# Performance work log

Measured on AMD Instinct MI355X. Metric: run time of the kernel, lower is better.

## Reference

```python
import jax, jax.numpy as jnp
import numpy as np
import math

N_S = 4096
N_T = 4096
R = 0.05
SIGMA = 0.2
K = 100.0
T = 1.0
S_MAX = 300.0
B = 100.0
ALPHA_STR = 30.0
CHI = 6.0
LAMBDA_PDE = 1.0
LAMBDA_BC = 10.0
LAMBDA_TC = 10.0
HUBER_DELTA = 0.01
ALPHA = 2.0 * R / SIGMA ** 2            # 2r/sigma^2
TAU_MAX = 0.5 * SIGMA ** 2 * T
DU = 1.0 / (N_S - 1)                     # dS_norm for the S-stencils
DT_NORM = TAU_MAX / (N_T - 1)            # dt_norm for the t-stencil


def _solve_depressed_cubic(Q):
    # Faithful port of CubicStretching._solve_depressed_cubic (hyperbolic root formula).
    p = CHI
    q = CHI * Q
    sp = math.sqrt(p)
    arg = abs(q) / (2.0 * p * sp / (3.0 * math.sqrt(3.0)))
    arg = max(1.0, arg)
    c = 2.0 * sp * math.cosh(math.acosh(arg) / 3.0)
    return -c if q >= 0 else c


C1 = _solve_depressed_cubic((B - 0.0) / ALPHA_STR)
C2 = _solve_depressed_cubic((B - S_MAX) / ALPHA_STR)


def _stretch_metrics(u):
    # CubicStretching.compute_metrics: S(u), dS/du, d2S/du2.
    L = C2 * u + C1 * (1.0 - u)
    dL = C2 - C1
    S = B + ALPHA_STR * (L ** 3 / CHI + L)
    dS = ALPHA_STR * dL * (0.5 * L ** 2 + 1.0)
    d2S = ALPHA_STR * dL ** 2 * L
    return S, dS, d2S


def setup_inputs() -> dict:
    key = jax.random.key(0)
    V_norm = 0.1 * jax.random.normal(key, (1, 1, N_S, N_T), dtype=jnp.float32)
    return {"V_norm": V_norm}


def reference(V_norm):
    # u-grid along S (axis 2), t-grid along time (axis 3)
    u = jnp.linspace(0.0, 1.0, N_S, dtype=jnp.float32)[None, None, :, None]  # [1,1,N_S,1]
    t = jnp.linspace(0.0, 1.0, N_T, dtype=jnp.float32)                       # [N_T]

    S_phys, S_u, S_uu = _stretch_metrics(u)
    S_norm = S_phys / S_MAX       # stretched physical coordinate, normalized
    S_u_n = S_u / S_MAX
    S_uu_n = S_uu / S_MAX

    # FD stencils: (3,1) central diff / second diff along S, (1,3) central diff along t,
    # all with replicate padding (= torch padding_mode='replicate').
    Vp = jnp.pad(V_norm, ((0, 0), (0, 0), (1, 1), (0, 0)), mode='edge')
    V_u = (Vp[:, :, 2:, :] - Vp[:, :, :-2, :]) / (2.0 * DU)
    V_uu = (Vp[:, :, 2:, :] - 2.0 * V_norm + Vp[:, :, :-2, :]) / DU ** 2
    Vt = jnp.pad(V_norm, ((0, 0), (0, 0), (0, 0), (1, 1)), mode='edge')
    V_t = (Vt[:, :, :, 2:] - Vt[:, :, :, :-2]) / (2.0 * DT_NORM)

    # Chain rule from uniform u to stretched S
    V_S = V_u / S_u_n
    V_SS = (V_uu * S_u_n - V_u * S_uu_n) / S_u_n ** 3
    V_SS = jnp.clip(V_SS, -100.0, 100.0)

    residual = V_t - S_norm ** 2 * V_SS - ALPHA * S_norm * V_S + ALPHA * V_norm
    # interior mask = relu(1 - S0 - Smax - T - t0) == strict interior of the grid
    n_int = (N_S - 2) * (N_T - 2)
    pde_loss = jnp.sum(residual[:, :, 1:-1, 1:-1] ** 2) / n_int

    # far-field BC at S = S_max (row N_S-1): call option -> 1 - K exp(-r(1-t))/S_max
    bc_target = 1.0 - K * jnp.exp(-R * (1.0 - t)) / S_MAX
    loss_Smax = jnp.sum((V_norm[0, 0, -1, :] - bc_target) ** 2) / N_T

    # terminal condition at t = T (col N_t-1): softplus payoff on the UNIFORM u grid
    # (forward rebinds S_norm = self.S_grid_norm before calling terminal_payoff)
    payoff = jax.nn.softplus(50.0 * (u[0, 0, :, 0] - K / S_MAX)) / 50.0
    diff_T = V_norm[0, 0, :, -1] - payoff
    abs_d = jnp.abs(diff_T)
    loss_T = jnp.sum(jnp.where(abs_d < HUBER_DELTA,
                               0.5 * diff_T ** 2,
                               HUBER_DELTA * (abs_d - 0.5 * HUBER_DELTA))) / N_S

    total = LAMBDA_PDE * pde_loss + LAMBDA_BC * loss_Smax + LAMBDA_TC * loss_T
    return total
```

## Files before the change

kernel.cpp:

```cpp
#include <hip/hip_runtime.h>
#include <math.h>

#define NS 4096
#define NT 4096
#define RPB 4
#define NBLK (NS / RPB)

__device__ __forceinline__ double block_reduce(double v, int tid) {
    #pragma unroll
    for (int off = 32; off > 0; off >>= 1)
        v += __shfl_down(v, off, 64);
    __shared__ double lds[4];
    const int lane = tid & 63, wv = tid >> 6;
    if (lane == 0) lds[wv] = v;
    __syncthreads();
    return lds[0] + lds[1] + lds[2] + lds[3];
}

__device__ __forceinline__ void load16(const float* __restrict__ p, float* d) {
    const float4 x0 = *(const float4*)(p);
    const float4 x1 = *(const float4*)(p + 4);
    const float4 x2 = *(const float4*)(p + 8);
    const float4 x3 = *(const float4*)(p + 12);
    d[0]=x0.x; d[1]=x0.y; d[2]=x0.z;  d[3]=x0.w;
    d[4]=x1.x; d[5]=x1.y; d[6]=x1.z;  d[7]=x1.w;
    d[8]=x2.x; d[9]=x2.y; d[10]=x2.z; d[11]=x2.w;
    d[12]=x3.x;d[13]=x3.y;d[14]=x3.z; d[15]=x3.w;
}

__global__ __launch_bounds__(256) void bs_main(const float* __restrict__ V,
                                               double* __restrict__ part,
                                               double C1, double C2) {
    const int tid = threadIdx.x;
    const int r0  = blockIdx.x * RPB;
    const int j0  = tid * 16;

    const double DU = 1.0 / (double)(NS - 1);
    const double dL = C2 - C1;

    const float INV2DU = 2047.5f;
    const float INVDU2 = 16769025.0f;
    const float INV2DT = 102375.0f;
    const float AL     = 2.5f;

    float a[16], b[16], c[16];
    const int rm = (r0 > 0) ? r0 - 1 : 0;
    load16(V + (size_t)rm * NT + j0, a);
    load16(V + (size_t)r0 * NT + j0, b);

    double pde = 0.0, bc = 0.0, tc = 0.0;

    #pragma unroll
    for (int rr = 0; rr < RPB; ++rr) {
        const int r  = r0 + rr;
        const int rn = (r + 1 < NS) ? r + 1 : NS - 1;
        load16(V + (size_t)rn * NT + j0, c);

        const double u   = (double)r * DU;
        const double L   = C2 * u + C1 * (1.0 - u);
        const double S   = 100.0 + 30.0 * (L * L * L / 6.0 + L);
        const double dS  = 30.0 * dL * (0.5 * L * L + 1.0);
        const double d2S = 30.0 * dL * dL * L;
        const float Sn   = (float)(S   / 300.0);
        const float Sun  = (float)(dS  / 300.0);
        const float Suun = (float)(d2S / 300.0);
        const float invSun  = 1.0f / Sun;
        const float invSun3 = invSun * invSun * invSun;
        const float Sn2 = Sn * Sn;
        const float ASn = AL * Sn;

        if (r >= 1 && r <= NS - 2) {
            const float lf = (j0 > 0)       ? V[(size_t)r * NT + j0 - 1]  : 0.0f;
            const float rt = (j0 + 16 < NT) ? V[(size_t)r * NT + j0 + 16] : 0.0f;

            float pf = 0.0f;
            #pragma unroll
            for (int k = 0; k < 16; ++k) {
                const int j = j0 + k;
                if (j >= 1 && j <= NT - 2) {
                    const float cm = (k == 0)  ? lf : b[k - 1];
                    const float cp = (k == 15) ? rt : b[k + 1];
                    const float Vu  = (c[k] - a[k]) * INV2DU;
                    const float Vuu = (c[k] - 2.0f * b[k] + a[k]) * INVDU2;
                    const float Vt  = (cp - cm) * INV2DT;
                    const float VS  = Vu * invSun;
                    float VSS = (Vuu * Sun - Vu * Suun) * invSun3;
                    VSS = fminf(fmaxf(VSS, -100.0f), 100.0f);
                    const float res = Vt - Sn2 * VSS - ASn * VS + AL * b[k];
                    pf += res * res;
                }
            }
            pde += (double)pf;
        }

        if (r == NS - 1) {
            #pragma unroll
            for (int k = 0; k < 16; ++k) {
                const float t   = (float)(j0 + k) * (1.0f / (float)(NT - 1));
                const float tgt = 1.0f - (100.0f / 300.0f) * expf(-0.05f * (1.0f - t));
                const float d   = b[k] - tgt;
                bc += (double)(d * d);
            }
        }

        if (tid == 255) {
            const float ui = (float)u;
            const float x  = 50.0f * (ui - 100.0f / 300.0f);
            const float sp = fmaxf(x, 0.0f) + log1pf(expf(-fabsf(x)));
            const float payoff = sp * (1.0f / 50.0f);
            const float d  = b[15] - payoff;
            const float ad = fabsf(d);
            tc += (double)((ad < 0.01f) ? 0.5f * d * d : 0.01f * (ad - 0.005f));
        }

        #pragma unroll
        for (int k = 0; k < 16; ++k) { a[k] = b[k]; b[k] = c[k]; }
    }

    const double n_int = (double)(NS - 2) * (double)(NT - 2);
    double contrib = pde * (1.0 / n_int)
                   + bc  * (10.0 / (double)NT)
                   + tc  * (10.0 / (double)NS);

    contrib = block_reduce(contrib, tid);
    if (tid == 0) part[blockIdx.x] = contrib;
}

__global__ __launch_bounds__(256) void bs_final(const double* __restrict__ part,
                                                float* __restrict__ out) {
    const int tid = threadIdx.x;
    double s = 0.0;
    for (int idx = tid; idx < NBLK; idx += 256) s += part[idx];
    s = block_reduce(s, tid);
    if (tid == 0) out[0] = (float)s;
}

static double cubic_root_host(double Q) {
    const double p = 6.0;
    const double q = p * Q;
    const double sp = sqrt(p);
    double arg = fabs(q) / (2.0 * p * sp / (3.0 * sqrt(3.0)));
    if (arg < 1.0) arg = 1.0;
    const double c = 2.0 * sp * cosh(acosh(arg) / 3.0);
    return (q >= 0.0) ? -c : c;
}

extern "C" void kernel_launch(void* const* d_in, const int* in_sizes, int n_in,
                              void* d_out, int out_size, void* d_ws, size_t ws_size,
                              hipStream_t stream) {
    const float* V  = (const float*)d_in[0];
    float* out      = (float*)d_out;
    double* part    = (double*)d_ws;

    const double C1 = cubic_root_host((100.0 - 0.0)   / 30.0);
    const double C2 = cubic_root_host((100.0 - 300.0) / 30.0);

    bs_main <<<NBLK, 256, 0, stream>>>(V, part, C1, C2);
    bs_final<<<1,    256, 0, stream>>>(part, out);
}
```

Measured before the change: 100.1 us.

## Split columns across blocks and fuse final reduction via last-block atomic counter

Each block now covers 8 rows and half of the columns, with 8 columns per thread instead of 16, so the grid stays at 1024 blocks while each thread holds less register data. The separate final reduction kernel is replaced by a last-block-done pattern using an atomic counter, with the counter reset by a memset before launch. This removes one kernel launch but adds a memset node and the serialized tail reduction in the last block. Halo loads per element rise slightly because each thread's column span is narrower.

New measurement: 125.4 us. +25.2%, slower.

```diff
diff --git a/kernel.cpp b/kernel.cpp
--- a/kernel.cpp
+++ b/kernel.cpp
@@ -3,8 +3,10 @@
 
 #define NS 4096
 #define NT 4096
-#define RPB 4
-#define NBLK (NS / RPB)
+#define RPB 8
+#define CCH 2048
+#define CPT 8
+#define NBLK ((NS / RPB) * (NT / CCH))
 
 __device__ __forceinline__ double block_reduce(double v, int tid) {
     #pragma unroll
@@ -17,23 +19,23 @@
     return lds[0] + lds[1] + lds[2] + lds[3];
 }
 
-__device__ __forceinline__ void load16(const float* __restrict__ p, float* d) {
+__device__ __forceinline__ void load8(const float* __restrict__ p, float* d) {
     const float4 x0 = *(const float4*)(p);
     const float4 x1 = *(const float4*)(p + 4);
-    const float4 x2 = *(const float4*)(p + 8);
-    const float4 x3 = *(const float4*)(p + 12);
-    d[0]=x0.x; d[1]=x0.y; d[2]=x0.z;  d[3]=x0.w;
-    d[4]=x1.x; d[5]=x1.y; d[6]=x1.z;  d[7]=x1.w;
-    d[8]=x2.x; d[9]=x2.y; d[10]=x2.z; d[11]=x2.w;
-    d[12]=x3.x;d[13]=x3.y;d[14]=x3.z; d[15]=x3.w;
+    d[0]=x0.x; d[1]=x0.y; d[2]=x0.z; d[3]=x0.w;
+    d[4]=x1.x; d[5]=x1.y; d[6]=x1.z; d[7]=x1.w;
 }
 
 __global__ __launch_bounds__(256) void bs_main(const float* __restrict__ V,
                                                double* __restrict__ part,
+                                               unsigned* __restrict__ cnt,
+                                               float* __restrict__ out,
                                                double C1, double C2) {
     const int tid = threadIdx.x;
-    const int r0  = blockIdx.x * RPB;
-    const int j0  = tid * 16;
+    const int rg  = blockIdx.x >> 1;
+    const int cc  = blockIdx.x & 1;
+    const int r0  = rg * RPB;
+    const int j0  = cc * CCH + tid * CPT;
 
     const double DU = 1.0 / (double)(NS - 1);
     const double dL = C2 - C1;
@@ -43,10 +45,10 @@
     const float INV2DT = 102375.0f;
     const float AL     = 2.5f;
 
-    float a[16], b[16], c[16];
+    float a[CPT], b[CPT], c[CPT];
     const int rm = (r0 > 0) ? r0 - 1 : 0;
-    load16(V + (size_t)rm * NT + j0, a);
-    load16(V + (size_t)r0 * NT + j0, b);
+    load8(V + (size_t)rm * NT + j0, a);
+    load8(V + (size_t)r0 * NT + j0, b);
 
     double pde = 0.0, bc = 0.0, tc = 0.0;
 
@@ -54,7 +56,7 @@
     for (int rr = 0; rr < RPB; ++rr) {
         const int r  = r0 + rr;
         const int rn = (r + 1 < NS) ? r + 1 : NS - 1;
-        load16(V + (size_t)rn * NT + j0, c);
+        load8(V + (size_t)rn * NT + j0, c);
 
         const double u   = (double)r * DU;
         const double L   = C2 * u + C1 * (1.0 - u);
@@ -70,16 +72,16 @@
         const float ASn = AL * Sn;
 
         if (r >= 1 && r <= NS - 2) {
-            const float lf = (j0 > 0)       ? V[(size_t)r * NT + j0 - 1]  : 0.0f;
-            const float rt = (j0 + 16 < NT) ? V[(size_t)r * NT + j0 + 16] : 0.0f;
+            const float lf = (j0 > 0)        ? V[(size_t)r * NT + j0 - 1]   : 0.0f;
+            const float rt = (j0 + CPT < NT) ? V[(size_t)r * NT + j0 + CPT] : 0.0f;
 
             float pf = 0.0f;
             #pragma unroll
-            for (int k = 0; k < 16; ++k) {
+            for (int k = 0; k < CPT; ++k) {
                 const int j = j0 + k;
                 if (j >= 1 && j <= NT - 2) {
-                    const float cm = (k == 0)  ? lf : b[k - 1];
-                    const float cp = (k == 15) ? rt : b[k + 1];
+                    const float cm = (k == 0)       ? lf : b[k - 1];
+                    const float cp = (k == CPT - 1) ? rt : b[k + 1];
                     const float Vu  = (c[k] - a[k]) * INV2DU;
                     const float Vuu = (c[k] - 2.0f * b[k] + a[k]) * INVDU2;
                     const float Vt  = (cp - cm) * INV2DT;
@@ -95,7 +97,7 @@
 
         if (r == NS - 1) {
             #pragma unroll
-            for (int k = 0; k < 16; ++k) {
+            for (int k = 0; k < CPT; ++k) {
                 const float t   = (float)(j0 + k) * (1.0f / (float)(NT - 1));
                 const float tgt = 1.0f - (100.0f / 300.0f) * expf(-0.05f * (1.0f - t));
                 const float d   = b[k] - tgt;
@@ -103,18 +105,18 @@
             }
         }
 
-        if (tid == 255) {
+        if (j0 + CPT == NT) {
             const float ui = (float)u;
             const float x  = 50.0f * (ui - 100.0f / 300.0f);
             const float sp = fmaxf(x, 0.0f) + log1pf(expf(-fabsf(x)));
             const float payoff = sp * (1.0f / 50.0f);
-            const float d  = b[15] - payoff;
+            const float d  = b[CPT - 1] - payoff;
             const float ad = fabsf(d);
             tc += (double)((ad < 0.01f) ? 0.5f * d * d : 0.01f * (ad - 0.005f));
         }
 
         #pragma unroll
-        for (int k = 0; k < 16; ++k) { a[k] = b[k]; b[k] = c[k]; }
+        for (int k = 0; k < CPT; ++k) { a[k] = b[k]; b[k] = c[k]; }
     }
 
     const double n_int = (double)(NS - 2) * (double)(NT - 2);
@@ -123,16 +125,23 @@
                    + tc  * (10.0 / (double)NS);
 
     contrib = block_reduce(contrib, tid);
-    if (tid == 0) part[blockIdx.x] = contrib;
-}
 
-__global__ __launch_bounds__(256) void bs_final(const double* __restrict__ part,
-                                                float* __restrict__ out) {
-    const int tid = threadIdx.x;
-    double s = 0.0;
-    for (int idx = tid; idx < NBLK; idx += 256) s += part[idx];
-    s = block_reduce(s, tid);
-    if (tid == 0) out[0] = (float)s;
+    __shared__ int amLast;
+    if (tid == 0) {
+        part[blockIdx.x] = contrib;
+        __threadfence();
+        const unsigned old = atomicAdd(cnt, 1u);
+        amLast = (old == (unsigned)(NBLK - 1));
+    }
+    __syncthreads();
+
+    if (amLast) {
+        double s = 0.0;
+        for (int idx = tid; idx < NBLK; idx += 256)
+            s += atomicAdd(&part[idx], 0.0);
+        s = block_reduce(s, tid);
+        if (tid == 0) out[0] = (float)s;
+    }
 }
 
 static double cubic_root_host(double Q) {
@@ -151,10 +160,11 @@
     const float* V  = (const float*)d_in[0];
     float* out      = (float*)d_out;
     double* part    = (double*)d_ws;
+    unsigned* cnt   = (unsigned*)((char*)d_ws + NBLK * sizeof(double));
 
     const double C1 = cubic_root_host((100.0 - 0.0)   / 30.0);
     const double C2 = cubic_root_host((100.0 - 300.0) / 30.0);
 
-    bs_main <<<NBLK, 256, 0, stream>>>(V, part, C1, C2);
-    bs_final<<<1,    256, 0, stream>>>(part, out);
+    hipMemsetAsync(cnt, 0, sizeof(unsigned), stream);
+    bs_main<<<NBLK, 256, 0, stream>>>(V, part, cnt, out, C1, C2);
 }
```
